# Kernel tuning notes

Hardware: AMD Instinct MI355X
Metric: run time of the kernel (lower is better)

## Reference

```python
import jax, jax.numpy as jnp
import numpy as np
from jax import lax

V, D, H, T = 50000, 300, 256, 34  # vocab, embed/input dim, lstm hidden, tags
B, S = 64, 256


def setup_inputs() -> dict:
    key = jax.random.key(0)
    ks = jax.random.split(key, 12)
    sc = 0.05
    inp = {
        "batch": jax.random.randint(ks[0], (B, S), 0, V),
        "tags": jax.random.randint(ks[1], (B, S), 0, T),
        "seq_lengths": jnp.full((B,), S, dtype=jnp.int64 if jax.config.jax_enable_x64 else jnp.int32),
        "emb": jax.random.normal(ks[2], (V, D), jnp.float32) * sc,
        "w_ih_f": jax.random.normal(ks[3], (4 * H, D), jnp.float32) * sc,
        "w_hh_f": jax.random.normal(ks[4], (4 * H, H), jnp.float32) * sc,
        "b_f": jnp.zeros((4 * H,), jnp.float32),
        "w_ih_b": jax.random.normal(ks[5], (4 * H, D), jnp.float32) * sc,
        "w_hh_b": jax.random.normal(ks[6], (4 * H, H), jnp.float32) * sc,
        "b_b": jnp.zeros((4 * H,), jnp.float32),
        "w_out": jax.random.normal(ks[7], (T, 2 * H), jnp.float32) * sc,
        "b_out": jnp.zeros((T,), jnp.float32),
        "start_t": jax.random.uniform(ks[8], (T,), jnp.float32, -0.1, 0.1),
        "end_t": jax.random.uniform(ks[9], (T,), jnp.float32, -0.1, 0.1),
        "trans": jax.random.uniform(ks[10], (T, T), jnp.float32, -0.1, 0.1),
    }
    return inp


def _lstm_dir(x_sbd, w_ih, w_hh, b, reverse):
    # x_sbd: [S,B,D]. Precompute input projections for all steps (one big GEMM).
    xg = jnp.einsum('sbd,gd->sbg', x_sbd, w_ih) + b  # [S,B,4H]
    h0 = jnp.zeros((x_sbd.shape[1], H), x_sbd.dtype)

    def step(carry, xg_t):
        h, c = carry
        g = xg_t + h @ w_hh.T  # [B,4H]; torch gate order i,f,g,o
        i, f, gg, o = jnp.split(g, 4, axis=-1)
        c = jax.nn.sigmoid(f) * c + jax.nn.sigmoid(i) * jnp.tanh(gg)
        h = jax.nn.sigmoid(o) * jnp.tanh(c)
        return (h, c), h

    _, hs = lax.scan(step, (h0, h0), xg, reverse=reverse)
    return hs  # [S,B,H]


def _crf_nll(emissions, tags, start_t, end_t, trans):
    # emissions [B,S,T], tags [B,S]; mask is all ones (see notes).
    b_idx = jnp.arange(emissions.shape[0])
    # numerator: score of the gold path
    em = jnp.take_along_axis(emissions, tags[:, :, None], axis=2)[..., 0].sum(axis=1)
    tr = trans[tags[:, :-1], tags[:, 1:]].sum(axis=1)
    num = start_t[tags[:, 0]] + em + tr + end_t[tags[:, -1]]
    # denominator: forward algorithm (log-sum-exp recurrence)
    em_sbt = jnp.swapaxes(emissions, 0, 1)  # [S,B,T]
    alpha0 = start_t[None, :] + em_sbt[0]  # [B,T]

    def step(alpha, emit_t):
        alpha = jax.nn.logsumexp(alpha[:, :, None] + trans[None, :, :], axis=1) + emit_t
        return alpha, None

    alpha, _ = lax.scan(step, alpha0, em_sbt[1:])
    den = jax.nn.logsumexp(alpha + end_t[None, :], axis=1)
    llh = num - den  # log-likelihood per sequence
    return -jnp.mean(llh)


def reference(batch, tags, seq_lengths, emb, w_ih_f, w_hh_f, b_f,
              w_ih_b, w_hh_b, b_b, w_out, b_out, start_t, end_t, trans):
    x = emb[batch]                       # [B,S,D] embedding lookup
    x_sbd = jnp.swapaxes(x, 0, 1)        # [S,B,D]
    hf = _lstm_dir(x_sbd, w_ih_f, w_hh_f, b_f, reverse=False)
    hb = _lstm_dir(x_sbd, w_ih_b, w_hh_b, b_b, reverse=True)
    hidden = jnp.concatenate([hf, hb], axis=-1)          # [S,B,2H]
    emit = jnp.einsum('sbh,th->bst', hidden, w_out) + b_out  # [B,S,T]
    # dropout is identity at eval (deterministic reference)
    return _crf_nll(emit, tags, start_t, end_t, trans)
```

## Files before the change

kernel.cpp:

```cpp
#include <hip/hip_runtime.h>

typedef short s8v __attribute__((ext_vector_type(8)));
typedef float f4v __attribute__((ext_vector_type(4)));
typedef unsigned short u16;
typedef unsigned char u8;
typedef long ll;

constexpr int MB = 64, SS = 256, DD = 300, DP = 320, HH = 256, TT = 34, TP = 48;
constexpr int MM = MB * SS;

constexpr size_t OFF_XBF  = 0;
constexpr size_t OFF_WIH  = OFF_XBF  + (size_t)MM * DP * 2;
constexpr size_t OFF_WHH8 = OFF_WIH  + (size_t)2048 * DP * 2;
constexpr size_t OFF_WOUT = OFF_WHH8 + (size_t)2048 * HH;
constexpr size_t OFF_XG   = OFF_WOUT + (size_t)TP * 512 * 2;
constexpr size_t OFF_HID  = OFF_XG   + (size_t)2 * 4 * 256 * 1024 * 16 * 2;
constexpr size_t OFF_EM   = OFF_HID  + (size_t)MM * 512 * 2;
constexpr size_t OFF_LLH  = OFF_EM   + (size_t)MM * 36 * 4;

__device__ inline u16 f2bf(float f) {
  unsigned u = __builtin_bit_cast(unsigned, f);
  unsigned r = u + 0x7fffu + ((u >> 16) & 1u);
  return (u16)(r >> 16);
}
__device__ inline float bf2f(u16 h) {
  return __builtin_bit_cast(float, (unsigned)h << 16);
}
__device__ inline float sigf(float x) { return __fdividef(1.f, 1.f + __expf(-x)); }
__device__ inline float tanhf_(float x) {
  float e = __expf(2.f * x);
  return __fdividef(e - 1.f, e + 1.f);
}
__device__ inline u8 f2fp8(float f) {
  unsigned v;
  asm("v_cvt_pk_fp8_f32 %0, %1, %2" : "=v"(v) : "v"(f), "v"(f));
  return (u8)(v & 0xff);
}

constexpr int XBF_CH = MM * (DP / 8);
constexpr int WIH_CH = 2048 * (DP / 8);
constexpr int WHH_CH = 2048 * (HH / 8);
constexpr int WOUT_CH = TP * (512 / 8);
constexpr int TOT_CH = XBF_CH + WIH_CH + WHH_CH + WOUT_CH;

__global__ __launch_bounds__(256) void k_prep(
    const int* __restrict__ batch, const float* __restrict__ emb,
    const float* __restrict__ wihf, const float* __restrict__ wihb,
    const float* __restrict__ whhf, const float* __restrict__ whhb,
    const float* __restrict__ wout,
    u16* __restrict__ xbf, u16* __restrict__ wih,
    u8* __restrict__ whh8, u16* __restrict__ wob) {
  int cid = blockIdx.x * 256 + threadIdx.x;
  if (cid >= TOT_CH) return;
  union { u16 u[8]; uint4 v; } pk;
  if (cid < XBF_CH) {
    int m = cid / 40, cc = cid - m * 40, d0 = cc * 8;
    int b = m & 63, s = m >> 6;
    int tok = batch[b * SS + s];
    const float* src = emb + (size_t)tok * DD;
    #pragma unroll
    for (int j = 0; j < 8; ++j) { int d = d0 + j; pk.u[j] = f2bf(d < DD ? src[d] : 0.f); }
    *(uint4*)(xbf + (size_t)m * DP + d0) = pk.v;
  } else if (cid < XBF_CH + WIH_CH) {
    int c2 = cid - XBF_CH;
    int row = c2 / 40, cc = c2 - row * 40, d0 = cc * 8;
    const float* src = row < 1024 ? (wihf + (size_t)row * DD) : (wihb + (size_t)(row - 1024) * DD);
    #pragma unroll
    for (int j = 0; j < 8; ++j) { int d = d0 + j; pk.u[j] = f2bf(d < DD ? src[d] : 0.f); }
    *(uint4*)(wih + (size_t)row * DP + d0) = pk.v;
  } else if (cid < XBF_CH + WIH_CH + WHH_CH) {
    int c2 = cid - (XBF_CH + WIH_CH);
    int row = c2 >> 5, d0 = (c2 & 31) * 8;
    const float* src = (row < 1024 ? whhf + (size_t)row * HH : whhb + (size_t)(row - 1024) * HH) + d0;
    unsigned q0, q1, q2, q3;
    asm("v_cvt_pk_fp8_f32 %0, %1, %2" : "=v"(q0) : "v"(src[0]), "v"(src[1]));
    asm("v_cvt_pk_fp8_f32 %0, %1, %2" : "=v"(q1) : "v"(src[2]), "v"(src[3]));
    asm("v_cvt_pk_fp8_f32 %0, %1, %2" : "=v"(q2) : "v"(src[4]), "v"(src[5]));
    asm("v_cvt_pk_fp8_f32 %0, %1, %2" : "=v"(q3) : "v"(src[6]), "v"(src[7]));
    uint2 o;
    o.x = (q0 & 0xffffu) | (q1 << 16);
    o.y = (q2 & 0xffffu) | (q3 << 16);
    *(uint2*)(whh8 + (size_t)row * HH + d0) = o;
  } else {
    int c2 = cid - (XBF_CH + WIH_CH + WHH_CH);
    int row = c2 >> 6, d0 = (c2 & 63) * 8;
    #pragma unroll
    for (int j = 0; j < 8; ++j) pk.u[j] = f2bf(row < TT ? wout[(size_t)row * 512 + d0 + j] : 0.f);
    *(uint4*)(wob + (size_t)row * 512 + d0) = pk.v;
  }
}

__global__ __launch_bounds__(256) void k_xg(
    const u16* __restrict__ xbf, const u16* __restrict__ wih,
    const float* __restrict__ bf_, const float* __restrict__ bb_,
    u16* __restrict__ xgt) {
  __shared__ u16 As[128][40];
  __shared__ u16 Bs[128][40];
  int m0 = blockIdx.x * 128, n0 = blockIdx.y * 128;
  int tid = threadIdx.x, lane = tid & 63, wid = tid >> 6;
  int wr = wid >> 1, wc = wid & 1;
  int r_lo = lane & 15, kc = (lane >> 4) * 8, row_hi = (lane >> 4) * 4;
  f4v acc[4][4] = {};
  for (int kt = 0; kt < 10; ++kt) {
    int k0 = kt * 32;
    #pragma unroll
    for (int i = 0; i < 2; ++i) {
      int cid = tid + 256 * i;
      int row = cid >> 2, cc = cid & 3;
      *(uint4*)(&As[row][cc * 8]) = *(const uint4*)(xbf + (size_t)(m0 + row) * DP + k0 + cc * 8);
      *(uint4*)(&Bs[row][cc * 8]) = *(const uint4*)(wih + (size_t)(n0 + row) * DP + k0 + cc * 8);
    }
    __syncthreads();
    s8v af[4], bfr[4];
    #pragma unroll
    for (int mi = 0; mi < 4; ++mi) af[mi] = *(const s8v*)(&As[wr * 64 + mi * 16 + r_lo][kc]);
    #pragma unroll
    for (int ni = 0; ni < 4; ++ni) bfr[ni] = *(const s8v*)(&Bs[wc * 64 + ni * 16 + r_lo][kc]);
    #pragma unroll
    for (int mi = 0; mi < 4; ++mi)
      #pragma unroll
      for (int ni = 0; ni < 4; ++ni)
        acc[mi][ni] = __builtin_amdgcn_mfma_f32_16x16x32_bf16(af[mi], bfr[ni], acc[mi][ni], 0, 0, 0);
    __syncthreads();
  }
  int s = (m0 + wr * 64) >> 6;
  #pragma unroll
  for (int mi = 0; mi < 4; ++mi)
    #pragma unroll
    for (int ni = 0; ni < 4; ++ni) {
      int n2 = n0 + wc * 64 + ni * 16 + r_lo;
      float bias = n2 < 1024 ? bf_[n2] : bb_[n2 - 1024];
      int dir = n2 >> 10, n = n2 & 1023;
      union { u16 u[4]; ll v; } pk4;
      #pragma unroll
      for (int r = 0; r < 4; ++r) pk4.u[r] = f2bf(acc[mi][ni][r] + bias);
      *(ll*)(xgt + ((((size_t)dir * 4 + mi) * 256 + s) * 1024 + n) * 16 + row_hi) = pk4.v;
    }
}

__global__ __launch_bounds__(512, 2) void k_lstm(
    const u16* __restrict__ xgt, const u8* __restrict__ whh8,
    u16* __restrict__ hidden) {
  __shared__ u8 hs[2][16 * 256];
  int wg = blockIdx.x, dir = wg >> 2, bg = wg & 3;
  int tid = threadIdx.x, lane = tid & 63, w = tid >> 6;
  int r_lo = lane & 15, hi = lane >> 4;

  ll wf[8][8];
  const u8* wb = whh8 + (size_t)dir * 1024 * 256;
  #pragma unroll
  for (int g = 0; g < 4; ++g)
    #pragma unroll
    for (int ut = 0; ut < 2; ++ut) {
      const u8* rp = wb + (size_t)(g * 256 + w * 32 + ut * 16 + r_lo) * 256 + hi * 8;
      #pragma unroll
      for (int kt = 0; kt < 8; ++kt)
        wf[g * 2 + ut][kt] = *(const ll*)(rp + kt * 32);
    }
  for (int i = tid; i < 2 * 16 * 256 / 4; i += 512) ((int*)hs)[i] = 0;
  float c[8];
  #pragma unroll
  for (int i = 0; i < 8; ++i) c[i] = 0.f;

  const u16* xbase = xgt + (((size_t)(dir * 4 + bg) * 256) * 1024 + w * 32) * 16;
  ll xb[8];
  {
    int s0 = dir ? 255 : 0;
    #pragma unroll
    for (int g = 0; g < 4; ++g)
      #pragma unroll
      for (int ut = 0; ut < 2; ++ut)
        xb[g * 2 + ut] = *(const ll*)(xbase + ((size_t)s0 * 1024 + g * 256 + ut * 16 + r_lo) * 16 + hi * 4);
  }
  __syncthreads();

  u16* hidb = hidden + (size_t)(bg * 16) * 512 + dir * 256 + w * 32;
  for (int step = 0; step < 256; ++step) {
    int s = dir ? 255 - step : step;
    f4v acc[8];
    #pragma unroll
    for (int nt = 0; nt < 8; ++nt) {
      unsigned lo = (unsigned)(unsigned long)xb[nt];
      unsigned h32 = (unsigned)(((unsigned long)xb[nt]) >> 32);
      acc[nt][0] = bf2f((u16)(lo & 0xffff));
      acc[nt][1] = bf2f((u16)(lo >> 16));
      acc[nt][2] = bf2f((u16)(h32 & 0xffff));
      acc[nt][3] = bf2f((u16)(h32 >> 16));
    }
    if (step < 255) {
      int sn = dir ? 254 - step : step + 1;
      #pragma unroll
      for (int g = 0; g < 4; ++g)
        #pragma unroll
        for (int ut = 0; ut < 2; ++ut)
          xb[g * 2 + ut] = *(const ll*)(xbase + ((size_t)sn * 1024 + g * 256 + ut * 16 + r_lo) * 16 + hi * 4);
    }
    const u8* hp = hs[step & 1];
    ll av[8];
    #pragma unroll
    for (int kt = 0; kt < 8; ++kt)
      av[kt] = *(const ll*)(hp + r_lo * 256 + ((kt * 32 + hi * 8) ^ (r_lo << 3)));
    #pragma unroll
    for (int kt = 0; kt < 8; ++kt)
      #pragma unroll
      for (int nt = 0; nt < 8; ++nt)
        acc[nt] = __builtin_amdgcn_mfma_f32_16x16x32_fp8_fp8(av[kt], wf[nt][kt], acc[nt], 0, 0, 0);
    u8* hq = hs[(step + 1) & 1];
    u16* hrow = hidb + (size_t)s * 64 * 512;
    #pragma unroll
    for (int q = 0; q < 4; ++q) {
      int b = hi * 4 + q;
      #pragma unroll
      for (int ut = 0; ut < 2; ++ut) {
        float gi = acc[0 + ut][q], gf = acc[2 + ut][q];
        float gg = acc[4 + ut][q], go = acc[6 + ut][q];
        float cv = sigf(gf) * c[q * 2 + ut] + sigf(gi) * tanhf_(gg);
        c[q * 2 + ut] = cv;
        float hv = sigf(go) * tanhf_(cv);
        hq[b * 256 + ((w * 32 + ut * 16 + r_lo) ^ (b << 3))] = f2fp8(hv);
        hrow[(size_t)b * 512 + ut * 16 + r_lo] = f2bf(hv);
      }
    }
    __syncthreads();
  }
}

__global__ __launch_bounds__(64) void k_emit(
    const u16* __restrict__ hidden, const u16* __restrict__ wob,
    const float* __restrict__ bout, float* __restrict__ em) {
  int m0 = blockIdx.x * 16;
  int lane = threadIdx.x;
  int r_lo = lane & 15, kc = (lane >> 4) * 8, row_hi = (lane >> 4) * 4;
  f4v acc[3] = {};
  #pragma unroll
  for (int kt = 0; kt < 16; ++kt) {
    int k0 = kt * 32 + kc;
    s8v a = *(const s8v*)(hidden + (size_t)(m0 + r_lo) * 512 + k0);
    #pragma unroll
    for (int nt = 0; nt < 3; ++nt) {
      s8v b = *(const s8v*)(wob + (size_t)(nt * 16 + r_lo) * 512 + k0);
      acc[nt] = __builtin_amdgcn_mfma_f32_16x16x32_bf16(a, b, acc[nt], 0, 0, 0);
    }
  }
  #pragma unroll
  for (int nt = 0; nt < 3; ++nt) {
    int t = nt * 16 + r_lo;
    if (t < TT) {
      float bo = bout[t];
      #pragma unroll
      for (int r = 0; r < 4; ++r)
        em[(size_t)(m0 + row_hi + r) * 36 + t] = acc[nt][r] + bo;
    }
  }
}

__global__ __launch_bounds__(64) void k_crf(
    const float* __restrict__ em, const int* __restrict__ tags,
    const float* __restrict__ startt, const float* __restrict__ endt,
    const float* __restrict__ trans, float* __restrict__ llh) {
  __shared__ float tr[34][35];
  __shared__ float al[2][40];
  int b = blockIdx.x, l = threadIdx.x;
  for (int i = l; i < TT * TT; i += 64) tr[i / TT][i - (i / TT) * TT] = trans[i];
  const int* tg = tags + b * SS;
  float np = 0.f;
  for (int s = l; s < SS; s += 64) {
    int t = tg[s];
    np += em[(size_t)(s * 64 + b) * 36 + t];
    if (s < SS - 1) np += trans[t * TT + tg[s + 1]];
  }
  #pragma unroll
  for (int o = 32; o; o >>= 1) np += __shfl_down(np, o, 64);
  float num = 0.f;
  if (l == 0) num = np + startt[tg[0]] + endt[tg[SS - 1]];
  if (l < TT) al[0][l] = startt[l] + em[(size_t)(0 * 64 + b) * 36 + l];
  __syncthreads();
  for (int s = 1; s < SS; ++s) {
    int p = s & 1;
    if (l < TT) {
      float m = -1e30f;
      for (int t = 0; t < TT; ++t) m = fmaxf(m, al[p ^ 1][t] + tr[t][l]);
      float sum = 0.f;
      for (int t = 0; t < TT; ++t) sum += __expf(al[p ^ 1][t] + tr[t][l] - m);
      al[p][l] = m + __logf(sum) + em[(size_t)(s * 64 + b) * 36 + l];
    }
    __syncthreads();
  }
  if (l == 0) {
    int p = (SS - 1) & 1;
    float m = -1e30f;
    for (int t = 0; t < TT; ++t) m = fmaxf(m, al[p][t] + endt[t]);
    float sum = 0.f;
    for (int t = 0; t < TT; ++t) sum += __expf(al[p][t] + endt[t] - m);
    llh[b] = num - (m + __logf(sum));
  }
}

__global__ __launch_bounds__(64) void k_red(const float* __restrict__ llh, float* __restrict__ out) {
  float v = llh[threadIdx.x];
  #pragma unroll
  for (int o = 32; o; o >>= 1) v += __shfl_down(v, o, 64);
  if (threadIdx.x == 0) out[0] = -v * (1.f / 64.f);
}

extern "C" void kernel_launch(void* const* d_in, const int* in_sizes, int n_in,
                              void* d_out, int out_size, void* d_ws, size_t ws_size,
                              hipStream_t stream) {
  const int* batch = (const int*)d_in[0];
  const int* tags = (const int*)d_in[1];
  const float* emb = (const float*)d_in[3];
  const float* wihf = (const float*)d_in[4];
  const float* whhf = (const float*)d_in[5];
  const float* bf_ = (const float*)d_in[6];
  const float* wihb = (const float*)d_in[7];
  const float* whhb = (const float*)d_in[8];
  const float* bb_ = (const float*)d_in[9];
  const float* wout = (const float*)d_in[10];
  const float* bout = (const float*)d_in[11];
  const float* startt = (const float*)d_in[12];
  const float* endt = (const float*)d_in[13];
  const float* trans = (const float*)d_in[14];

  char* ws = (char*)d_ws;
  u16* xbf  = (u16*)(ws + OFF_XBF);
  u16* wih  = (u16*)(ws + OFF_WIH);
  u8*  whh8 = (u8*)(ws + OFF_WHH8);
  u16* wob  = (u16*)(ws + OFF_WOUT);
  u16* xgt  = (u16*)(ws + OFF_XG);
  u16* hid  = (u16*)(ws + OFF_HID);
  float* em = (float*)(ws + OFF_EM);
  float* llh = (float*)(ws + OFF_LLH);
  float* out = (float*)d_out;

  k_prep<<<(TOT_CH + 255) / 256, 256, 0, stream>>>(batch, emb, wihf, wihb, whhf, whhb, wout,
                                                   xbf, wih, whh8, wob);
  k_xg<<<dim3(MM / 128, 2048 / 128), 256, 0, stream>>>(xbf, wih, bf_, bb_, xgt);
  k_lstm<<<8, 512, 0, stream>>>(xgt, whh8, hid);
  k_emit<<<MM / 16, 64, 0, stream>>>(hid, wob, bout, em);
  k_crf<<<64, 64, 0, stream>>>(em, tags, startt, endt, trans, llh);
  k_red<<<1, 64, 0, stream>>>(llh, out);
}
```

Before: 1.373 ms.

## Split LSTM step MFMAs into two halves, overlap prefetch and lighten barrier

Reorders the recurrent LSTM step so the h-fragment LDS reads come first and the MFMAs run in two groups of four accumulators. The next step's xgate prefetch is issued between the two groups, and each group's gate math is done separately, which shortens accumulator live ranges and lets loads overlap compute. It also swaps __syncthreads for an explicit lgkmcnt wait plus s_barrier, uses pointer-increment addressing with cheaper bf16 unpacking, and unrolls the CRF logsumexp loop with two accumulators. The risks are added register pressure and relying on the custom barrier for correct ordering of LDS writes.

```diff
diff --git a/kernel.cpp b/kernel.cpp
--- a/kernel.cpp
+++ b/kernel.cpp
@@ -35,6 +35,14 @@
   unsigned v;
   asm("v_cvt_pk_fp8_f32 %0, %1, %2" : "=v"(v) : "v"(f), "v"(f));
   return (u8)(v & 0xff);
+}
+__device__ inline f4v unpk(unsigned lo, unsigned hi32) {
+  f4v r;
+  r[0] = __builtin_bit_cast(float, lo << 16);
+  r[1] = __builtin_bit_cast(float, lo & 0xffff0000u);
+  r[2] = __builtin_bit_cast(float, hi32 << 16);
+  r[3] = __builtin_bit_cast(float, hi32 & 0xffff0000u);
+  return r;
 }
 
 constexpr int XBF_CH = MM * (DP / 8);
@@ -157,71 +165,84 @@
       for (int kt = 0; kt < 8; ++kt)
         wf[g * 2 + ut][kt] = *(const ll*)(rp + kt * 32);
     }
-  for (int i = tid; i < 2 * 16 * 256 / 4; i += 512) ((int*)hs)[i] = 0;
+  for (int i = tid; i < 16 * 256 / 4; i += 512) ((int*)hs[0])[i] = 0;
   float c[8];
   #pragma unroll
   for (int i = 0; i < 8; ++i) c[i] = 0.f;
 
-  const u16* xbase = xgt + (((size_t)(dir * 4 + bg) * 256) * 1024 + w * 32) * 16;
-  ll xb[8];
-  {
-    int s0 = dir ? 255 : 0;
-    #pragma unroll
-    for (int g = 0; g < 4; ++g)
-      #pragma unroll
-      for (int ut = 0; ut < 2; ++ut)
-        xb[g * 2 + ut] = *(const ll*)(xbase + ((size_t)s0 * 1024 + g * 256 + ut * 16 + r_lo) * 16 + hi * 4);
-  }
+  const u16* xptr = xgt + (((size_t)(dir * 4 + bg) * 256 + (dir ? 255 : 0)) * 1024 + w * 32) * 16;
+  const long xstep = dir ? -(1024 * 16) : (1024 * 16);
+  unsigned xb[8][2];
+  #pragma unroll
+  for (int g = 0; g < 4; ++g)
+    #pragma unroll
+    for (int ut = 0; ut < 2; ++ut) {
+      uint2 v = *(const uint2*)(xptr + ((size_t)g * 256 + ut * 16 + r_lo) * 16 + hi * 4);
+      xb[g * 2 + ut][0] = v.x; xb[g * 2 + ut][1] = v.y;
+    }
+  u16* hptr = hidden + ((size_t)(dir ? 255 : 0) * 64 + bg * 16) * 512 + dir * 256 + w * 32;
+  const long hstep = dir ? -(64 * 512) : (64 * 512);
   __syncthreads();
 
-  u16* hidb = hidden + (size_t)(bg * 16) * 512 + dir * 256 + w * 32;
   for (int step = 0; step < 256; ++step) {
-    int s = dir ? 255 - step : step;
-    f4v acc[8];
-    #pragma unroll
-    for (int nt = 0; nt < 8; ++nt) {
-      unsigned lo = (unsigned)(unsigned long)xb[nt];
-      unsigned h32 = (unsigned)(((unsigned long)xb[nt]) >> 32);
-      acc[nt][0] = bf2f((u16)(lo & 0xffff));
-      acc[nt][1] = bf2f((u16)(lo >> 16));
-      acc[nt][2] = bf2f((u16)(h32 & 0xffff));
-      acc[nt][3] = bf2f((u16)(h32 >> 16));
-    }
+    const u8* hp = hs[step & 1];
+    ll av[8];
+    #pragma unroll
+    for (int kt = 0; kt < 8; ++kt)
+      av[kt] = *(const ll*)(hp + r_lo * 256 + ((kt * 32 + hi * 8) ^ (r_lo << 3)));
+    f4v a0 = unpk(xb[0][0], xb[0][1]);
+    f4v a1 = unpk(xb[2][0], xb[2][1]);
+    f4v a2 = unpk(xb[4][0], xb[4][1]);
+    f4v a3 = unpk(xb[6][0], xb[6][1]);
+    #pragma unroll
+    for (int kt = 0; kt < 8; ++kt) {
+      a0 = __builtin_amdgcn_mfma_f32_16x16x32_fp8_fp8(av[kt], wf[0][kt], a0, 0, 0, 0);
+      a1 = __builtin_amdgcn_mfma_f32_16x16x32_fp8_fp8(av[kt], wf[2][kt], a1, 0, 0, 0);
+      a2 = __builtin_amdgcn_mfma_f32_16x16x32_fp8_fp8(av[kt], wf[4][kt], a2, 0, 0, 0);
+      a3 = __builtin_amdgcn_mfma_f32_16x16x32_fp8_fp8(av[kt], wf[6][kt], a3, 0, 0, 0);
+    }
+    f4v b0 = unpk(xb[1][0], xb[1][1]);
+    f4v b1 = unpk(xb[3][0], xb[3][1]);
+    f4v b2 = unpk(xb[5][0], xb[5][1]);
+    f4v b3 = unpk(xb[7][0], xb[7][1]);
     if (step < 255) {
-      int sn = dir ? 254 - step : step + 1;
+      xptr += xstep;
       #pragma unroll
       for (int g = 0; g < 4; ++g)
         #pragma unroll
-        for (int ut = 0; ut < 2; ++ut)
-          xb[g * 2 + ut] = *(const ll*)(xbase + ((size_t)sn * 1024 + g * 256 + ut * 16 + r_lo) * 16 + hi * 4);
-    }
-    const u8* hp = hs[step & 1];
-    ll av[8];
-    #pragma unroll
-    for (int kt = 0; kt < 8; ++kt)
-      av[kt] = *(const ll*)(hp + r_lo * 256 + ((kt * 32 + hi * 8) ^ (r_lo << 3)));
-    #pragma unroll
-    for (int kt = 0; kt < 8; ++kt)
-      #pragma unroll
-      for (int nt = 0; nt < 8; ++nt)
-        acc[nt] = __builtin_amdgcn_mfma_f32_16x16x32_fp8_fp8(av[kt], wf[nt][kt], acc[nt], 0, 0, 0);
+        for (int ut = 0; ut < 2; ++ut) {
+          uint2 v = *(const uint2*)(xptr + ((size_t)g * 256 + ut * 16 + r_lo) * 16 + hi * 4);
+          xb[g * 2 + ut][0] = v.x; xb[g * 2 + ut][1] = v.y;
+        }
+    }
+    #pragma unroll
+    for (int kt = 0; kt < 8; ++kt) {
+      b0 = __builtin_amdgcn_mfma_f32_16x16x32_fp8_fp8(av[kt], wf[1][kt], b0, 0, 0, 0);
+      b1 = __builtin_amdgcn_mfma_f32_16x16x32_fp8_fp8(av[kt], wf[3][kt], b1, 0, 0, 0);
+      b2 = __builtin_amdgcn_mfma_f32_16x16x32_fp8_fp8(av[kt], wf[5][kt], b2, 0, 0, 0);
+      b3 = __builtin_amdgcn_mfma_f32_16x16x32_fp8_fp8(av[kt], wf[7][kt], b3, 0, 0, 0);
+    }
     u8* hq = hs[(step + 1) & 1];
-    u16* hrow = hidb + (size_t)s * 64 * 512;
     #pragma unroll
     for (int q = 0; q < 4; ++q) {
       int b = hi * 4 + q;
-      #pragma unroll
-      for (int ut = 0; ut < 2; ++ut) {
-        float gi = acc[0 + ut][q], gf = acc[2 + ut][q];
-        float gg = acc[4 + ut][q], go = acc[6 + ut][q];
-        float cv = sigf(gf) * c[q * 2 + ut] + sigf(gi) * tanhf_(gg);
-        c[q * 2 + ut] = cv;
-        float hv = sigf(go) * tanhf_(cv);
-        hq[b * 256 + ((w * 32 + ut * 16 + r_lo) ^ (b << 3))] = f2fp8(hv);
-        hrow[(size_t)b * 512 + ut * 16 + r_lo] = f2bf(hv);
-      }
-    }
-    __syncthreads();
+      float cv = sigf(a1[q]) * c[q * 2] + sigf(a0[q]) * tanhf_(a2[q]);
+      c[q * 2] = cv;
+      float hv = sigf(a3[q]) * tanhf_(cv);
+      hq[b * 256 + ((w * 32 + r_lo) ^ (b << 3))] = f2fp8(hv);
+      hptr[(size_t)b * 512 + r_lo] = f2bf(hv);
+    }
+    #pragma unroll
+    for (int q = 0; q < 4; ++q) {
+      int b = hi * 4 + q;
+      float cv = sigf(b1[q]) * c[q * 2 + 1] + sigf(b0[q]) * tanhf_(b2[q]);
+      c[q * 2 + 1] = cv;
+      float hv = sigf(b3[q]) * tanhf_(cv);
+      hq[b * 256 + ((w * 32 + 16 + r_lo) ^ (b << 3))] = f2fp8(hv);
+      hptr[(size_t)b * 512 + 16 + r_lo] = f2bf(hv);
+    }
+    hptr += hstep;
+    asm volatile("s_waitcnt lgkmcnt(0)\n\ts_barrier" ::: "memory");
   }
 }
 
@@ -278,11 +299,20 @@
   for (int s = 1; s < SS; ++s) {
     int p = s & 1;
     if (l < TT) {
-      float m = -1e30f;
-      for (int t = 0; t < TT; ++t) m = fmaxf(m, al[p ^ 1][t] + tr[t][l]);
-      float sum = 0.f;
-      for (int t = 0; t < TT; ++t) sum += __expf(al[p ^ 1][t] + tr[t][l] - m);
-      al[p][l] = m + __logf(sum) + em[(size_t)(s * 64 + b) * 36 + l];
+      float m0 = -1e30f, m1 = -1e30f;
+      #pragma unroll
+      for (int t = 0; t < TT; t += 2) {
+        m0 = fmaxf(m0, al[p ^ 1][t] + tr[t][l]);
+        m1 = fmaxf(m1, al[p ^ 1][t + 1] + tr[t + 1][l]);
+      }
+      float m = fmaxf(m0, m1);
+      float s0 = 0.f, s1 = 0.f;
+      #pragma unroll
+      for (int t = 0; t < TT; t += 2) {
+        s0 += __expf(al[p ^ 1][t] + tr[t][l] - m);
+        s1 += __expf(al[p ^ 1][t + 1] + tr[t + 1][l] - m);
+      }
+      al[p][l] = m + __logf(s0 + s1) + em[(size_t)(s * 64 + b) * 36 + l];
     }
     __syncthreads();
   }
```

New measurement: 1.174 ms. -14.5%, faster.
